# Performance work log

Hardware: AMD Instinct MI355X
Metric: run time of the kernel (lower is better)

The kernel has to match this reference:

```python
import jax, jax.numpy as jnp
import numpy as np

V, E, H, Z = 32000, 512, 1024, 256
B, S, T = 64, 256, 64
BOS_ID, EOS_ID = 1, 2


def gru_cell(x_gates, h, W_hh, b_hh):
    # torch GRU gate order: r, z, n. x_gates: (B,3H) precomputed W_ih@x+b_ih.
    hg = h @ W_hh.T + b_hh
    xr, xz, xn = jnp.split(x_gates, 3, axis=-1)
    hr, hz, hn = jnp.split(hg, 3, axis=-1)
    r = jax.nn.sigmoid(xr + hr)
    z = jax.nn.sigmoid(xz + hz)
    n = jnp.tanh(xn + r * hn)
    return (1.0 - z) * n + z * h


def setup_inputs() -> dict:
    key = jax.random.key(0)
    ks = jax.random.split(key, 24)
    u = lambda k, sh: jax.random.uniform(k, sh, jnp.float32, -0.1, 0.1)
    n = lambda k, sh: jax.random.normal(k, sh, jnp.float32) * 0.05
    inp = {
        'input': jax.random.randint(ks[0], (S, B), 0, V),
        'eps': jax.random.normal(ks[1], (B, Z), jnp.float32),
        'emb_enc': u(ks[2], (V, E)).at[0].set(0.0),  # padding_idx=0
        'Wih_e': n(ks[3], (3 * H, E)), 'Whh_e': n(ks[4], (3 * H, H)),
        'bih_e': n(ks[5], (3 * H,)), 'bhh_e': n(ks[6], (3 * H,)),
        'W_enc': n(ks[7], (Z, H)), 'b_enc': n(ks[8], (Z,)),
        'W_loc': n(ks[9], (Z, Z)), 'b_loc': n(ks[10], (Z,)),
        'W_scale': n(ks[11], (Z, Z)), 'b_scale': n(ks[12], (Z,)),
        'emb_dec': u(ks[13], (V, E)).at[0].set(0.0),
        'W_dec': n(ks[14], (H, Z)), 'b_dec': n(ks[15], (H,)),
        'Wih_d': n(ks[16], (3 * H, E)), 'Whh_d': n(ks[17], (3 * H, H)),
        'bih_d': n(ks[18], (3 * H,)), 'bhh_d': n(ks[19], (3 * H,)),
        'W_voc': n(ks[20], (V, H)), 'b_voc': n(ks[21], (V,)),
    }
    return inp


def reference(input, eps, emb_enc, Wih_e, Whh_e, bih_e, bhh_e,
              W_enc, b_enc, W_loc, b_loc, W_scale, b_scale,
              emb_dec, W_dec, b_dec, Wih_d, Whh_d, bih_d, bhh_d,
              W_voc, b_voc):
    # ---- encode ----
    x = emb_enc[input]                                   # (S,B,E)
    gx = jnp.einsum('sbe,ge->sbg', x, Wih_e) + bih_e     # (S,B,3H)
    h0 = jnp.zeros((B, H), x.dtype)
    h_last, _ = jax.lax.scan(lambda h, g: (gru_cell(g, h, Whh_e, bhh_e), None), h0, gx)
    henc = h_last @ W_enc.T + b_enc                      # (B,Z)
    loc = henc @ W_loc.T + b_loc
    scale = jax.nn.softplus(henc @ W_scale.T + b_scale)
    # ---- reparametrize ----
    z = loc + eps * jnp.exp(0.5 * scale)
    # ---- decode (fixed T steps; original loop is data-dependent on EOS) ----
    hidden = z @ W_dec.T + b_dec                         # (B,H)
    xd = jnp.broadcast_to(emb_dec[EOS_ID], (B, E))       # constant EOS input each step
    gxd = xd @ Wih_d.T + bih_d                           # (B,3H), hoisted out of loop

    def step(h, _):
        h2 = gru_cell(gxd, h, Whh_d, bhh_d)
        log_p = jax.nn.log_softmax(h2 @ W_voc.T + b_voc, axis=-1)  # (B,V)
        tok = jnp.argmax(log_p)  # global flat argmax, as torch.argmax(...).item()
        return h2, (log_p, tok)

    _, (log_p, toks) = jax.lax.scan(step, hidden, None, length=T)
    seq = jnp.concatenate([jnp.array([BOS_ID], toks.dtype), toks])
    return log_p, seq, loc, scale
```

## Files before the change

kernel.cpp:

```cpp
#include <hip/hip_runtime.h>
#include <math.h>
#include <stdint.h>
#include <stddef.h>

typedef unsigned short u16;
typedef unsigned int   u32;
typedef __attribute__((ext_vector_type(8))) short short8;
typedef __attribute__((ext_vector_type(4))) float f32x4;

#define DI __device__ __forceinline__

static constexpr int Vv = 32000, Ee = 512, Hh = 1024, Zz = 256;
static constexpr int Bb = 64, Ss = 256, Tt = 64;
static constexpr int G3 = 3 * Hh;

static constexpr size_t OFF_WHHE  = 0;
static constexpr size_t SZ_WHH    = (size_t)G3 * Hh * 2;
static constexpr size_t OFF_WHHD  = OFF_WHHE + SZ_WHH;
static constexpr size_t OFF_WIHE3 = OFF_WHHD + SZ_WHH;
static constexpr size_t SZ_WIHE3  = (size_t)G3 * (3 * Ee) * 2;
static constexpr size_t OFF_WVOC  = OFF_WIHE3 + SZ_WIHE3;
static constexpr size_t SZ_WVOC   = (size_t)Vv * Hh * 2;
static constexpr size_t OFF_XS    = OFF_WVOC + SZ_WVOC;
static constexpr size_t SZ_XS     = (size_t)Ss * Bb * (3 * Ee) * 2;
static constexpr size_t OFF_GX    = OFF_XS + SZ_XS;
static constexpr size_t SZ_GX     = (size_t)Ss * Bb * G3 * 4;
static constexpr size_t OFF_H2B   = OFF_GX;
static constexpr size_t OFF_H2F   = OFF_GX + SZ_GX;
static constexpr size_t SZ_H2F    = (size_t)Tt * Bb * Hh * 4;
static constexpr size_t OFF_H     = OFF_H2F + SZ_H2F;
static constexpr size_t OFF_GXD   = OFF_H + (size_t)Bb * Hh * 4;
static constexpr size_t OFF_HENC  = OFF_GXD + 12288;
static constexpr size_t OFF_ZB    = OFF_HENC + (size_t)Bb * Zz * 4;
static constexpr size_t OFF_RM    = OFF_ZB + (size_t)Bb * Zz * 4;
static constexpr size_t OFF_SE    = OFF_RM + 16384;
static constexpr size_t OFF_LSE   = OFF_SE + 16384;
static constexpr size_t OFF_BV    = OFF_LSE + 16384;
static constexpr size_t OFF_BI    = OFF_BV + 16384;
static constexpr size_t OFF_CC    = OFF_BI + 16384;
static constexpr size_t OFF_CAND  = OFF_CC + 16384;
static constexpr size_t OFF_BAR   = OFF_CAND + (size_t)4096 * 32 * 4;

static constexpr size_t SZ_HAB    = (size_t)Bb * 2 * Hh * 2;

DI u16 f2bf(float f) {
  u32 u = __float_as_uint(f);
  u32 r = (u + 0x7FFFu + ((u >> 16) & 1u)) >> 16;
  return (u16)r;
}
DI float bf2f(u16 h) { return __uint_as_float(((u32)h) << 16); }

DI f32x4 mfma16(short8 a, short8 b, f32x4 c) {
  return __builtin_amdgcn_mfma_f32_16x16x32_bf16(a, b, c, 0, 0, 0);
}
DI void llds16(const u16* g, u16* l) {
  __builtin_amdgcn_global_load_lds(
      (const __attribute__((address_space(1))) u32*)g,
      (__attribute__((address_space(3))) u32*)l, 16, 0, 0);
}

DI void ag_store_u32(u32* p, u32 v) {
  __hip_atomic_store(p, v, __ATOMIC_RELAXED, __HIP_MEMORY_SCOPE_AGENT);
}
DI u32 ag_load_u32(const u32* p) {
  return __hip_atomic_load((u32*)p, __ATOMIC_RELAXED, __HIP_MEMORY_SCOPE_AGENT);
}
DI void ag_store_f32(float* p, float v) {
  __hip_atomic_store(p, v, __ATOMIC_RELAXED, __HIP_MEMORY_SCOPE_AGENT);
}

DI u16* hbuf_dev(char* rA, char* rB, char* rC, int i) {
  if (i < 192) return (u16*)(rA + (size_t)i * SZ_HAB);
  if (i < 228) return (u16*)(rB + (size_t)(i - 192) * SZ_HAB);
  return (u16*)(rC + (size_t)(i - 228) * SZ_HAB);
}

__global__ void k_zero(u32* p, int n) {
  for (int i = blockIdx.x * 256 + threadIdx.x; i < n; i += gridDim.x * 256) p[i] = 0;
}

__global__ void k_tobf(const float* __restrict__ W, u16* __restrict__ Wb, int n) {
  for (int i = blockIdx.x * 256 + threadIdx.x; i < n; i += gridDim.x * 256) Wb[i] = f2bf(W[i]);
}

__global__ void k_xgather(const int* __restrict__ inp, const float* __restrict__ emb,
                          u16* __restrict__ xs) {
  int n = Ss * Bb * Ee;
  for (int i = blockIdx.x * 256 + threadIdx.x; i < n; i += gridDim.x * 256) {
    int m = i >> 9, k = i & (Ee - 1);
    xs[i] = f2bf(emb[(size_t)inp[m] * Ee + k]);
  }
}

__global__ void k_gxd(const float* __restrict__ emb_dec, const float* __restrict__ Wih_d,
                      const float* __restrict__ bih_d, float* __restrict__ gxd) {
  int g = blockIdx.x * 256 + threadIdx.x;
  if (g >= G3) return;
  const float* er = emb_dec + 2 * Ee;
  const float* wr = Wih_d + (size_t)g * Ee;
  float s = 0.f;
  for (int e = 0; e < Ee; e++) s += er[e] * wr[e];
  gxd[g] = s + bih_d[g];
}

__global__ __launch_bounds__(256, 2) void gemm_bt(
    const u16* __restrict__ A, const u16* __restrict__ Bw, const float* __restrict__ bias,
    float* __restrict__ C, int M, int N, int K) {
  __shared__ __align__(16) u16 As[128 * 32];
  __shared__ __align__(16) u16 Bs[128 * 32];
  int tid = threadIdx.x;
  int wave = tid >> 6, lane = tid & 63;
  int wr = wave >> 1, wc = wave & 1;
  int m0 = blockIdx.y * 128, n0 = blockIdx.x * 128;
  f32x4 acc[4][4];
#pragma unroll
  for (int i = 0; i < 4; i++)
#pragma unroll
    for (int j = 0; j < 4; j++) acc[i][j] = (f32x4){0.f, 0.f, 0.f, 0.f};

  int lrow = lane >> 2, lcol = (lane & 3) * 8;
  int r15 = lane & 15, kk = (lane >> 4) * 8;

  for (int k0 = 0; k0 < K; k0 += 32) {
    __syncthreads();
#pragma unroll
    for (int rch = 0; rch < 2; rch++) {
      int c = rch * 4 + wave;
      int row = c * 16 + lrow;
      llds16(A  + (size_t)(m0 + row) * K + k0 + lcol, &As[c * 512]);
      llds16(Bw + (size_t)(n0 + row) * K + k0 + lcol, &Bs[c * 512]);
    }
    __syncthreads();
    short8 af[4], bfv[4];
#pragma unroll
    for (int mi = 0; mi < 4; mi++)
      af[mi] = *(const short8*)&As[(wr * 64 + mi * 16 + r15) * 32 + kk];
#pragma unroll
    for (int ni = 0; ni < 4; ni++)
      bfv[ni] = *(const short8*)&Bs[(wc * 64 + ni * 16 + r15) * 32 + kk];
#pragma unroll
    for (int mi = 0; mi < 4; mi++)
#pragma unroll
      for (int ni = 0; ni < 4; ni++) acc[mi][ni] = mfma16(af[mi], bfv[ni], acc[mi][ni]);
  }
#pragma unroll
  for (int mi = 0; mi < 4; mi++)
#pragma unroll
    for (int ni = 0; ni < 4; ni++) {
      int col = n0 + wc * 64 + ni * 16 + r15;
      float bs = bias[col];
#pragma unroll
      for (int i = 0; i < 4; i++) {
        int row = m0 + wr * 64 + mi * 16 + (lane >> 4) * 4 + i;
        C[(size_t)row * N + col] = acc[mi][ni][i] + bs;
      }
    }
}

template <int DEC>
__global__ __launch_bounds__(512, 1) void k_pers(
    const u16* __restrict__ W, const float* __restrict__ bhh, const float* __restrict__ gx0,
    char* rA, char* rB, char* rC, float* Hst, float* h2f0, u16* h2b0, u32* bar) {
  int tid = threadIdx.x, wave = tid >> 6, lane = tid & 63;
  int r15 = lane & 15, kk = (lane >> 4) * 8;
  int bq = blockIdx.x & 3, jt = blockIdx.x >> 2;
  int b0 = bq * 16, j0 = jt * 16;
  int kbase = wave * 128;
  const int NSTEP = DEC ? Tt : Ss;

  __shared__ float sC[8][64][13];
  __shared__ float hT[256];
  __shared__ __align__(8) u16 stg[2][16][16];

  int bl = tid >> 4, jc = tid & 15;
  float br = 0.f, bz = 0.f, bn = 0.f;
  float xr = 0.f, xz = 0.f, xn = 0.f;
  if (tid < 256) {
    hT[tid] = DEC ? Hst[(size_t)(b0 + bl) * Hh + j0 + jc] : 0.f;
    int j = j0 + jc;
    br = bhh[j]; bz = bhh[Hh + j]; bn = bhh[2 * Hh + j];
    if (DEC) { xr = gx0[j]; xz = gx0[Hh + j]; xn = gx0[2 * Hh + j]; }
    else {
      const float* gr = gx0 + (size_t)(b0 + bl) * G3;
      xr = gr[j]; xz = gr[Hh + j]; xn = gr[2 * Hh + j];
    }
  }
  __syncthreads();

  const u16* Wrow = W + (size_t)(j0 + r15) * Hh + kbase + kk;
  int lsrc = (bl >> 2) * 16 + jc;
  int isrc = bl & 3;
  int flgidx = (lane * 4 + bq) * 16;

  for (int st = 0; st < NSTEP; st++) {
    const u16* hin = hbuf_dev(rA, rB, rC, st);

    f32x4 acc[3];
#pragma unroll
    for (int g = 0; g < 3; g++) acc[g] = (f32x4){0.f, 0.f, 0.f, 0.f};
    const u16* Ab = hin + (size_t)(b0 + r15) * 2048 + kbase + kk;
#pragma unroll
    for (int ks = 0; ks < 4; ks++) {
      int ko = ks * 32;
      short8 ah = *(const short8*)(Ab + ko);
      short8 al = *(const short8*)(Ab + 1024 + ko);
      short8 w0 = *(const short8*)(Wrow + ko);
      short8 w1 = *(const short8*)(Wrow + (size_t)Hh * Hh + ko);
      short8 w2 = *(const short8*)(Wrow + (size_t)2 * Hh * Hh + ko);
      acc[0] = mfma16(ah, w0, acc[0]);
      acc[1] = mfma16(ah, w1, acc[1]);
      acc[2] = mfma16(ah, w2, acc[2]);
      acc[0] = mfma16(al, w0, acc[0]);
      acc[1] = mfma16(al, w1, acc[1]);
      acc[2] = mfma16(al, w2, acc[2]);
    }
#pragma unroll
    for (int g = 0; g < 3; g++)
#pragma unroll
      for (int i = 0; i < 4; i++) sC[wave][lane][g * 4 + i] = acc[g][i];
    __syncthreads();

    if (tid < 256) {
      float hgr = br, hgz = bz, hgn = bn;
#pragma unroll
      for (int w = 0; w < 8; w++) {
        hgr += sC[w][lsrc][isrc];
        hgz += sC[w][lsrc][4 + isrc];
        hgn += sC[w][lsrc][8 + isrc];
      }
      float rg = 1.0f / (1.0f + expf(-(xr + hgr)));
      float zg = 1.0f / (1.0f + expf(-(xz + hgz)));
      float ng = tanhf(xn + rg * hgn);
      float hn = (1.0f - zg) * ng + zg * hT[tid];
      hT[tid] = hn;
      u16 hi = f2bf(hn), lo = f2bf(hn - bf2f(hi));
      stg[0][bl][jc] = hi;
      stg[1][bl][jc] = lo;
      if (DEC) ag_store_f32(&h2f0[((size_t)st * Bb + b0 + bl) * Hh + j0 + jc], hn);
    }
    __syncthreads();

    if (tid < 256) {
      int part = tid >> 7, idx = tid & 127, row = idx >> 3, dw = idx & 7;
      if (st + 1 < NSTEP) {
        u16* hout = hbuf_dev(rA, rB, rC, st + 1);
        u32 val = ((const u32*)&stg[part][row][0])[dw];
        ag_store_u32((u32*)(hout + (size_t)(b0 + row) * 2048 + part * 1024 + j0) + dw, val);
      }
      if (DEC && tid < 128) {
        u16* h2b = h2b0 + (size_t)st * Bb * Hh;
        ag_store_u32((u32*)(h2b + (size_t)(b0 + row) * Hh + j0) + dw,
                     ((const u32*)&stg[0][row][0])[dw]);
      }
    }

    if (st + 1 < NSTEP) {
      asm volatile("s_waitcnt vmcnt(0)" ::: "memory");
      __syncthreads();
      if (tid == 0)
        ag_store_u32(&bar[blockIdx.x * 16], (u32)(st + 1));
      if (!DEC && tid < 256) {
        const float* gr = gx0 + ((size_t)(st + 1) * Bb + b0 + bl) * G3;
        int j = j0 + jc;
        xr = gr[j]; xz = gr[Hh + j]; xn = gr[2 * Hh + j];
      }
      for (;;) {
        int v = (int)ag_load_u32(&bar[flgidx]);
        if (__all(v >= st + 1)) break;
        __builtin_amdgcn_s_sleep(1);
      }
    }
  }

  if (!DEC && tid < 256)
    Hst[(size_t)(b0 + bl) * Hh + j0 + jc] = hT[tid];
}

template <int DEC>
__global__ __launch_bounds__(512, 1) void k_step3(
    const u16* __restrict__ W, const float* __restrict__ bhh, const float* __restrict__ gxp,
    const u16* __restrict__ hAin, u16* __restrict__ hAout, float* __restrict__ h,
    float* __restrict__ h2f, u16* __restrict__ h2b) {
  __shared__ float sC[4][64][13];
  int tid = threadIdx.x, wave = tid >> 6, lane = tid & 63;
  int mw = wave & 3, khalf = wave >> 2;
  int m0 = mw * 16;
  int r15 = lane & 15, kk = (lane >> 4) * 8;
  int j0 = blockIdx.x * 16;
  int kbase = khalf * 512;

  f32x4 acc[3];
#pragma unroll
  for (int g = 0; g < 3; g++) acc[g] = (f32x4){0.f, 0.f, 0.f, 0.f};

  const u16* Ah = hAin + (size_t)(m0 + r15) * 2048 + kbase + kk;
  const u16* Wr = W + (size_t)(j0 + r15) * Hh + kbase + kk;
#pragma unroll 4
  for (int ks = 0; ks < 16; ks++) {
    int ko = ks * 32;
    short8 ah = *(const short8*)(Ah + ko);
    short8 al = *(const short8*)(Ah + 1024 + ko);
    short8 b0 = *(const short8*)(Wr + ko);
    short8 b1 = *(const short8*)(Wr + (size_t)Hh * Hh + ko);
    short8 b2 = *(const short8*)(Wr + (size_t)2 * Hh * Hh + ko);
    acc[0] = mfma16(ah, b0, acc[0]);
    acc[1] = mfma16(ah, b1, acc[1]);
    acc[2] = mfma16(ah, b2, acc[2]);
    acc[0] = mfma16(al, b0, acc[0]);
    acc[1] = mfma16(al, b1, acc[1]);
    acc[2] = mfma16(al, b2, acc[2]);
  }

  if (khalf == 1) {
#pragma unroll
    for (int g = 0; g < 3; g++)
#pragma unroll
      for (int i = 0; i < 4; i++) sC[mw][lane][g * 4 + i] = acc[g][i];
  }
  __syncthreads();
  if (khalf == 1) return;

  int j = j0 + r15;
  float br = bhh[j], bz = bhh[Hh + j], bn = bhh[2 * Hh + j];
  float xrD = 0.f, xzD = 0.f, xnD = 0.f;
  if (DEC) { xrD = gxp[j]; xzD = gxp[Hh + j]; xnD = gxp[2 * Hh + j]; }
#pragma unroll
  for (int i = 0; i < 4; i++) {
    int b = m0 + (lane >> 4) * 4 + i;
    float hgr = acc[0][i] + sC[mw][lane][i]     + br;
    float hgz = acc[1][i] + sC[mw][lane][4 + i] + bz;
    float hgn = acc[2][i] + sC[mw][lane][8 + i] + bn;
    float xr, xz, xn;
    if (DEC) { xr = xrD; xz = xzD; xn = xnD; }
    else {
      const float* gr = gxp + (size_t)b * G3;
      xr = gr[j]; xz = gr[Hh + j]; xn = gr[2 * Hh + j];
    }
    float rg = 1.0f / (1.0f + expf(-(xr + hgr)));
    float zg = 1.0f / (1.0f + expf(-(xz + hgz)));
    float ng = tanhf(xn + rg * hgn);
    float hold = h[(size_t)b * Hh + j];
    float hn = (1.0f - zg) * ng + zg * hold;
    h[(size_t)b * Hh + j] = hn;
    u16 hi = f2bf(hn);
    u16 lo = f2bf(hn - bf2f(hi));
    hAout[(size_t)b * 2048 + j] = hi;
    hAout[(size_t)b * 2048 + 1024 + j] = lo;
    if (DEC) {
      h2f[(size_t)b * Hh + j] = hn;
      h2b[(size_t)b * Hh + j] = hi;
    }
  }
}

__global__ __launch_bounds__(256, 2) void k_head1(const float* __restrict__ h,
    const float* __restrict__ Wenc, const float* __restrict__ benc, float* __restrict__ henc) {
  int b = blockIdx.x;
  __shared__ float hs[Hh];
  for (int k = threadIdx.x; k < Hh; k += 256) hs[k] = h[(size_t)b * Hh + k];
  __syncthreads();
  int q = threadIdx.x;
  const float* wrw = Wenc + (size_t)q * Hh;
  float s = 0.f;
  for (int k = 0; k < Hh; k++) s += hs[k] * wrw[k];
  henc[b * Zz + q] = s + benc[q];
}

__global__ __launch_bounds__(256, 2) void k_head2(const float* __restrict__ henc,
    const float* __restrict__ Wloc, const float* __restrict__ bloc,
    const float* __restrict__ Wsc, const float* __restrict__ bsc,
    const float* __restrict__ eps, float* __restrict__ outLoc, float* __restrict__ outSc,
    float* __restrict__ zb) {
  int b = blockIdx.x;
  __shared__ float hs[Zz];
  if (threadIdx.x < Zz) hs[threadIdx.x] = henc[b * Zz + threadIdx.x];
  __syncthreads();
  int q = threadIdx.x;
  const float* wl = Wloc + (size_t)q * Zz;
  const float* wsp = Wsc + (size_t)q * Zz;
  float sl = 0.f, ssum = 0.f;
  for (int k = 0; k < Zz; k++) { sl += hs[k] * wl[k]; ssum += hs[k] * wsp[k]; }
  sl += bloc[q]; ssum += bsc[q];
  float sp = fmaxf(ssum, 0.f) + log1pf(expf(-fabsf(ssum)));
  float zv = sl + eps[b * Zz + q] * expf(0.5f * sp);
  outLoc[b * Zz + q] = sl;
  outSc[b * Zz + q] = sp;
  zb[b * Zz + q] = zv;
}

__global__ __launch_bounds__(256, 2) void k_head3(const float* __restrict__ zb,
    const float* __restrict__ Wdec, const float* __restrict__ bdec,
    float* __restrict__ h, u16* __restrict__ hA0) {
  int b = blockIdx.x;
  __shared__ float zs[Zz];
  if (threadIdx.x < Zz) zs[threadIdx.x] = zb[b * Zz + threadIdx.x];
  __syncthreads();
  for (int j = threadIdx.x; j < Hh; j += 256) {
    const float* wrw = Wdec + (size_t)j * Zz;
    float s = 0.f;
    for (int k = 0; k < Zz; k++) s += zs[k] * wrw[k];
    s += bdec[j];
    h[(size_t)b * Hh + j] = s;
    u16 hi = f2bf(s);
    u16 lo = f2bf(s - bf2f(hi));
    hA0[(size_t)b * 2048 + j] = hi;
    hA0[(size_t)b * 2048 + 1024 + j] = lo;
  }
}

__global__ __launch_bounds__(1024, 1) void k_soft(
    float* __restrict__ logits, const float* __restrict__ h2f,
    const float* __restrict__ Wvoc, const float* __restrict__ bvoc,
    float* __restrict__ bestv, int* __restrict__ besti) {
  __shared__ float row[Vv];
  __shared__ float hrow[Hh];
  __shared__ float red[16];
  __shared__ float srm, ssum, slse;
  __shared__ int lcnt, scc;
  __shared__ int lcand[32];
  __shared__ float lex[32], del[32];
  int r = blockIdx.x;
  int tid = threadIdx.x, wave = tid >> 6, lane = tid & 63;
  float* grow = logits + (size_t)r * Vv;
  if (tid == 0) lcnt = 0;
  hrow[tid] = h2f[(size_t)r * Hh + tid];
  float m = -3.0e38f;
  for (int c = tid * 4; c < Vv; c += 4096) {
    f32x4 v = *(const f32x4*)(grow + c);
    *(f32x4*)(row + c) = v;
    m = fmaxf(fmaxf(m, v.x), fmaxf(v.y, fmaxf(v.z, v.w)));
  }
  for (int o = 32; o; o >>= 1) m = fmaxf(m, __shfl_xor(m, o));
  if (lane == 0) red[wave] = m;
  __syncthreads();
  if (tid == 0) {
    float t = red[0];
    for (int i = 1; i < 16; i++) t = fmaxf(t, red[i]);
    srm = t;
  }
  __syncthreads();
  float rm = srm;
  float s = 0.f;
  for (int c = tid * 4; c < Vv; c += 4096) {
    f32x4 v = *(const f32x4*)(row + c);
    s += expf(v.x - rm) + expf(v.y - rm) + expf(v.z - rm) + expf(v.w - rm);
    if (v.x >= rm - 0.0625f) { int sl = atomicAdd(&lcnt, 1); if (sl < 32) lcand[sl] = c; }
    if (v.y >= rm - 0.0625f) { int sl = atomicAdd(&lcnt, 1); if (sl < 32) lcand[sl] = c + 1; }
    if (v.z >= rm - 0.0625f) { int sl = atomicAdd(&lcnt, 1); if (sl < 32) lcand[sl] = c + 2; }
    if (v.w >= rm - 0.0625f) { int sl = atomicAdd(&lcnt, 1); if (sl < 32) lcand[sl] = c + 3; }
  }
  for (int o = 32; o; o >>= 1) s += __shfl_xor(s, o);
  if (lane == 0) red[wave] = s;
  __syncthreads();
  if (tid == 0) {
    float t = 0.f;
    for (int i = 0; i < 16; i++) t += red[i];
    ssum = t;
    int cc = lcnt < 32 ? lcnt : 32;
    for (int i = 0; i < cc; i++)
      for (int k2 = i + 1; k2 < cc; k2++)
        if (lcand[k2] < lcand[i]) { int q = lcand[i]; lcand[i] = lcand[k2]; lcand[k2] = q; }
    scc = cc;
  }
  __syncthreads();
  int cnt = scc;
  for (int ci = wave; ci < cnt; ci += 16) {
    int v = lcand[ci];
    const float* wrw = Wvoc + (size_t)v * Hh;
    float sd = 0.f;
    for (int k = lane; k < Hh; k += 64) sd += hrow[k] * wrw[k];
    for (int o = 32; o; o >>= 1) sd += __shfl_xor(sd, o);
    if (lane == 0) {
      float le = sd + bvoc[v];
      lex[ci] = le;
      del[ci] = expf(le - rm) - expf(row[v] - rm);
    }
  }
  __syncthreads();
  if (tid == 0) {
    float se = ssum;
    for (int i = 0; i < cnt; i++) se += del[i];
    float lse = rm + logf(se);
    slse = lse;
    float bv = -3.0e38f; int bvi = 0;
    for (int i = 0; i < cnt; i++)
      if (lex[i] > bv) { bv = lex[i]; bvi = lcand[i]; }
    bestv[r] = bv - lse;
    besti[r] = (r & 63) * Vv + bvi;
  }
  __syncthreads();
  float l = slse;
  for (int c = tid * 4; c < Vv; c += 4096) {
    f32x4 v = *(const f32x4*)(row + c);
    v.x -= l; v.y -= l; v.z -= l; v.w -= l;
    *(f32x4*)(grow + c) = v;
  }
}

__global__ void k_argmax(const float* __restrict__ bestv, const int* __restrict__ besti,
                         float* __restrict__ outseq) {
  int tid = threadIdx.x;
  if (tid == 0) outseq[0] = 1.0f;
  for (int t = 0; t < Tt; t++) {
    float v = bestv[t * 64 + tid];
    int ii = besti[t * 64 + tid];
    for (int o = 1; o < 64; o <<= 1) {
      float ov = __shfl_xor(v, o);
      int oi = __shfl_xor(ii, o);
      if (ov > v || (ov == v && oi < ii)) { v = ov; ii = oi; }
    }
    if (tid == 0) outseq[1 + t] = (float)ii;
  }
}

extern "C" void kernel_launch(void* const* d_in, const int* in_sizes, int n_in,
                              void* d_out, int out_size, void* d_ws, size_t ws_size,
                              hipStream_t stream) {
  (void)in_sizes; (void)n_in; (void)out_size; (void)ws_size;
  const int*   inp     = (const int*)d_in[0];
  const float* eps     = (const float*)d_in[1];
  const float* emb_enc = (const float*)d_in[2];
  const float* Wih_e   = (const float*)d_in[3];
  const float* Whh_e   = (const float*)d_in[4];
  const float* bih_e   = (const float*)d_in[5];
  const float* bhh_e   = (const float*)d_in[6];
  const float* W_enc   = (const float*)d_in[7];
  const float* b_enc   = (const float*)d_in[8];
  const float* W_loc   = (const float*)d_in[9];
  const float* b_loc   = (const float*)d_in[10];
  const float* W_sc    = (const float*)d_in[11];
  const float* b_sc    = (const float*)d_in[12];
  const float* emb_dec = (const float*)d_in[13];
  const float* W_dec   = (const float*)d_in[14];
  const float* b_dec   = (const float*)d_in[15];
  const float* Wih_d   = (const float*)d_in[16];
  const float* Whh_d   = (const float*)d_in[17];
  const float* bih_d   = (const float*)d_in[18];
  const float* bhh_d   = (const float*)d_in[19];
  const float* W_voc   = (const float*)d_in[20];
  const float* b_voc   = (const float*)d_in[21];

  char* ws = (char*)d_ws;
  u16*   WHHE  = (u16*)(ws + OFF_WHHE);
  u16*   WHHD  = (u16*)(ws + OFF_WHHD);
  u16*   WIHB  = (u16*)(ws + OFF_WIHE3);
  u16*   WVOC  = (u16*)(ws + OFF_WVOC);
  u16*   XS    = (u16*)(ws + OFF_XS);
  float* GX    = (float*)(ws + OFF_GX);
  float* Hst   = (float*)(ws + OFF_H);
  float* H2F   = (float*)(ws + OFF_H2F);
  u16*   H2B   = (u16*)(ws + OFF_H2B);
  float* GXD   = (float*)(ws + OFF_GXD);
  float* HENC  = (float*)(ws + OFF_HENC);
  float* ZB    = (float*)(ws + OFF_ZB);
  float* BV    = (float*)(ws + OFF_BV);
  int*   BI    = (int*)(ws + OFF_BI);
  u32*   BAR   = (u32*)(ws + OFF_BAR);

  char* rA = ws + OFF_XS;
  char* rB = ws + OFF_WIHE3;
  char* rC = ws + OFF_H2F;
  auto hbuf = [&](int i) -> u16* {
    if (i < 192) return (u16*)(rA + (size_t)i * SZ_HAB);
    if (i < 228) return (u16*)(rB + (size_t)(i - 192) * SZ_HAB);
    return (u16*)(rC + (size_t)(i - 228) * SZ_HAB);
  };

  float* out     = (float*)d_out;
  float* logits  = out;
  float* outseq  = out + (size_t)Tt * Bb * Vv;
  float* outloc  = outseq + (Tt + 1);
  float* outsc   = outloc + Bb * Zz;

  k_tobf<<<1024, 256, 0, stream>>>(Whh_e, WHHE, G3 * Hh);
  k_tobf<<<1024, 256, 0, stream>>>(Whh_d, WHHD, G3 * Hh);
  k_tobf<<<512, 256, 0, stream>>>(Wih_e, WIHB, G3 * Ee);
  k_tobf<<<2048, 256, 0, stream>>>(W_voc, WVOC, Vv * Hh);
  k_xgather<<<2048, 256, 0, stream>>>(inp, emb_enc, XS);

  {
    dim3 g(G3 / 128, (Ss * Bb) / 128);
    gemm_bt<<<g, 256, 0, stream>>>(XS, WIHB, bih_e, GX, Ss * Bb, G3, Ee);
  }
  k_gxd<<<12, 256, 0, stream>>>(emb_dec, Wih_d, bih_d, GXD);
  k_zero<<<64, 256, 0, stream>>>((u32*)hbuf(0), (int)(SZ_HAB / 4));
  k_zero<<<1, 256, 0, stream>>>(BAR, 4096);

  hipError_t ce;
  {
    const u16* a0 = WHHE; const float* a1 = bhh_e; const float* a2 = GX;
    char* a3 = rA; char* a4 = rB; char* a5 = rC; float* a6 = Hst;
    float* a7 = nullptr; u16* a8 = nullptr; u32* a9 = BAR;
    void* args[] = {&a0,&a1,&a2,&a3,&a4,&a5,&a6,&a7,&a8,&a9};
    ce = hipLaunchCooperativeKernel(reinterpret_cast<void*>(&k_pers<0>),
                                    dim3(256), dim3(512), args, 0, stream);
  }
  if (ce != hipSuccess) {
    for (int s = 0; s < Ss; s++)
      k_step3<0><<<64, 512, 0, stream>>>(WHHE, bhh_e, GX + (size_t)s * Bb * G3,
                                         hbuf(s), hbuf(s + 1), Hst, nullptr, nullptr);
  }

  k_head1<<<64, 256, 0, stream>>>(Hst, W_enc, b_enc, HENC);
  k_head2<<<64, 256, 0, stream>>>(HENC, W_loc, b_loc, W_sc, b_sc, eps, outloc, outsc, ZB);
  k_head3<<<64, 256, 0, stream>>>(ZB, W_dec, b_dec, Hst, hbuf(0));
  k_zero<<<1, 256, 0, stream>>>(BAR, 4096);

  {
    const u16* a0 = WHHD; const float* a1 = bhh_d; const float* a2 = GXD;
    char* a3 = rA; char* a4 = rB; char* a5 = rC; float* a6 = Hst;
    float* a7 = H2F; u16* a8 = H2B; u32* a9 = BAR;
    void* args[] = {&a0,&a1,&a2,&a3,&a4,&a5,&a6,&a7,&a8,&a9};
    hipError_t cd = hipLaunchCooperativeKernel(reinterpret_cast<void*>(&k_pers<1>),
                                               dim3(256), dim3(512), args, 0, stream);
    if (cd != hipSuccess) {
      for (int t = 0; t < Tt; t++)
        k_step3<1><<<64, 512, 0, stream>>>(WHHD, bhh_d, GXD, hbuf(t), hbuf(t + 1), Hst,
                                           H2F + (size_t)t * Bb * Hh,
                                           H2B + (size_t)t * Bb * Hh);
    }
  }

  {
    dim3 g(Vv / 128, (Tt * Bb) / 128);
    gemm_bt<<<g, 256, 0, stream>>>(H2B, WVOC, b_voc, logits, Tt * Bb, Vv, Hh);
  }

  k_soft<<<Tt * Bb, 1024, 0, stream>>>(logits, H2F, W_voc, b_voc, BV, BI);
  k_argmax<<<1, 64, 0, stream>>>(BV, BI, outseq);
}
```

Before: 2.637 ms.

## Group vocab GEMM tiles for L2 reuse, drop LDS row cache in softmax, single-wave barrier poll

The vocab projection now runs as a new grouped-tile GEMM. Each run of consecutive blocks covers all M tiles for a group of 5 N tiles, so W_voc tiles are reused from L2 across the 32 row tiles. The softmax kernel no longer stages the 32000-float logits row in shared memory and instead re-reads it from global memory, which cuts LDS use so more blocks can be resident per CU. In the persistent GRU kernel, only wave 0 now spins on the grid barrier flag and the other waves wait at a block-level sync, which reduces polling traffic.

Result: faster. 2.576 ms (-2.3%).

```diff
diff --git a/kernel.cpp b/kernel.cpp
--- a/kernel.cpp
+++ b/kernel.cpp
@@ -32,14 +32,9 @@
 static constexpr size_t OFF_GXD   = OFF_H + (size_t)Bb * Hh * 4;
 static constexpr size_t OFF_HENC  = OFF_GXD + 12288;
 static constexpr size_t OFF_ZB    = OFF_HENC + (size_t)Bb * Zz * 4;
-static constexpr size_t OFF_RM    = OFF_ZB + (size_t)Bb * Zz * 4;
-static constexpr size_t OFF_SE    = OFF_RM + 16384;
-static constexpr size_t OFF_LSE   = OFF_SE + 16384;
-static constexpr size_t OFF_BV    = OFF_LSE + 16384;
+static constexpr size_t OFF_BV    = OFF_ZB + (size_t)Bb * Zz * 4;
 static constexpr size_t OFF_BI    = OFF_BV + 16384;
-static constexpr size_t OFF_CC    = OFF_BI + 16384;
-static constexpr size_t OFF_CAND  = OFF_CC + 16384;
-static constexpr size_t OFF_BAR   = OFF_CAND + (size_t)4096 * 32 * 4;
+static constexpr size_t OFF_BAR   = OFF_BI + 16384;
 
 static constexpr size_t SZ_HAB    = (size_t)Bb * 2 * Hh * 2;
 
@@ -112,6 +107,65 @@
   int wave = tid >> 6, lane = tid & 63;
   int wr = wave >> 1, wc = wave & 1;
   int m0 = blockIdx.y * 128, n0 = blockIdx.x * 128;
+  f32x4 acc[4][4];
+#pragma unroll
+  for (int i = 0; i < 4; i++)
+#pragma unroll
+    for (int j = 0; j < 4; j++) acc[i][j] = (f32x4){0.f, 0.f, 0.f, 0.f};
+
+  int lrow = lane >> 2, lcol = (lane & 3) * 8;
+  int r15 = lane & 15, kk = (lane >> 4) * 8;
+
+  for (int k0 = 0; k0 < K; k0 += 32) {
+    __syncthreads();
+#pragma unroll
+    for (int rch = 0; rch < 2; rch++) {
+      int c = rch * 4 + wave;
+      int row = c * 16 + lrow;
+      llds16(A  + (size_t)(m0 + row) * K + k0 + lcol, &As[c * 512]);
+      llds16(Bw + (size_t)(n0 + row) * K + k0 + lcol, &Bs[c * 512]);
+    }
+    __syncthreads();
+    short8 af[4], bfv[4];
+#pragma unroll
+    for (int mi = 0; mi < 4; mi++)
+      af[mi] = *(const short8*)&As[(wr * 64 + mi * 16 + r15) * 32 + kk];
+#pragma unroll
+    for (int ni = 0; ni < 4; ni++)
+      bfv[ni] = *(const short8*)&Bs[(wc * 64 + ni * 16 + r15) * 32 + kk];
+#pragma unroll
+    for (int mi = 0; mi < 4; mi++)
+#pragma unroll
+      for (int ni = 0; ni < 4; ni++) acc[mi][ni] = mfma16(af[mi], bfv[ni], acc[mi][ni]);
+  }
+#pragma unroll
+  for (int mi = 0; mi < 4; mi++)
+#pragma unroll
+    for (int ni = 0; ni < 4; ni++) {
+      int col = n0 + wc * 64 + ni * 16 + r15;
+      float bs = bias[col];
+#pragma unroll
+      for (int i = 0; i < 4; i++) {
+        int row = m0 + wr * 64 + mi * 16 + (lane >> 4) * 4 + i;
+        C[(size_t)row * N + col] = acc[mi][ni][i] + bs;
+      }
+    }
+}
+
+__global__ __launch_bounds__(256, 2) void gemm_grp(
+    const u16* __restrict__ A, const u16* __restrict__ Bw, const float* __restrict__ bias,
+    float* __restrict__ C, int M, int N, int K, int GN) {
+  __shared__ __align__(16) u16 As[128 * 32];
+  __shared__ __align__(16) u16 Bs[128 * 32];
+  int tid = threadIdx.x;
+  int wave = tid >> 6, lane = tid & 63;
+  int wr = wave >> 1, wc = wave & 1;
+  int mp = M >> 7;
+  int perg = mp * GN;
+  int grp = blockIdx.x / perg;
+  int rem = blockIdx.x - grp * perg;
+  int m0 = (rem / GN) * 128;
+  int n0 = (grp * GN + rem % GN) * 128;
   f32x4 acc[4][4];
 #pragma unroll
   for (int i = 0; i < 4; i++)
@@ -264,11 +318,14 @@
         int j = j0 + jc;
         xr = gr[j]; xz = gr[Hh + j]; xn = gr[2 * Hh + j];
       }
-      for (;;) {
-        int v = (int)ag_load_u32(&bar[flgidx]);
-        if (__all(v >= st + 1)) break;
-        __builtin_amdgcn_s_sleep(1);
+      if (wave == 0) {
+        for (;;) {
+          int v = (int)ag_load_u32(&bar[flgidx]);
+          if (__all(v >= st + 1)) break;
+          __builtin_amdgcn_s_sleep(1);
+        }
       }
+      __syncthreads();
     }
   }
 
@@ -408,11 +465,10 @@
   }
 }
 
-__global__ __launch_bounds__(1024, 1) void k_soft(
+__global__ __launch_bounds__(1024, 8) void k_soft(
     float* __restrict__ logits, const float* __restrict__ h2f,
     const float* __restrict__ Wvoc, const float* __restrict__ bvoc,
     float* __restrict__ bestv, int* __restrict__ besti) {
-  __shared__ float row[Vv];
   __shared__ float hrow[Hh];
   __shared__ float red[16];
   __shared__ float srm, ssum, slse;
@@ -427,7 +483,6 @@
   float m = -3.0e38f;
   for (int c = tid * 4; c < Vv; c += 4096) {
     f32x4 v = *(const f32x4*)(grow + c);
-    *(f32x4*)(row + c) = v;
     m = fmaxf(fmaxf(m, v.x), fmaxf(v.y, fmaxf(v.z, v.w)));
   }
   for (int o = 32; o; o >>= 1) m = fmaxf(m, __shfl_xor(m, o));
@@ -442,7 +497,7 @@
   float rm = srm;
   float s = 0.f;
   for (int c = tid * 4; c < Vv; c += 4096) {
-    f32x4 v = *(const f32x4*)(row + c);
+    f32x4 v = *(const f32x4*)(grow + c);
     s += expf(v.x - rm) + expf(v.y - rm) + expf(v.z - rm) + expf(v.w - rm);
     if (v.x >= rm - 0.0625f) { int sl = atomicAdd(&lcnt, 1); if (sl < 32) lcand[sl] = c; }
     if (v.y >= rm - 0.0625f) { int sl = atomicAdd(&lcnt, 1); if (sl < 32) lcand[sl] = c + 1; }
@@ -473,7 +528,7 @@
     if (lane == 0) {
       float le = sd + bvoc[v];
       lex[ci] = le;
-      del[ci] = expf(le - rm) - expf(row[v] - rm);
+      del[ci] = expf(le - rm) - expf(grow[v] - rm);
     }
   }
   __syncthreads();
@@ -491,7 +546,7 @@
   __syncthreads();
   float l = slse;
   for (int c = tid * 4; c < Vv; c += 4096) {
-    f32x4 v = *(const f32x4*)(row + c);
+    f32x4 v = *(const f32x4*)(grow + c);
     v.x -= l; v.y -= l; v.z -= l; v.w -= l;
     *(f32x4*)(grow + c) = v;
   }
@@ -621,10 +676,7 @@
     }
   }
 
-  {
-    dim3 g(Vv / 128, (Tt * Bb) / 128);
-    gemm_bt<<<g, 256, 0, stream>>>(H2B, WVOC, b_voc, logits, Tt * Bb, Vv, Hh);
-  }
+  gemm_grp<<<8000, 256, 0, stream>>>(H2B, WVOC, b_voc, logits, Tt * Bb, Vv, Hh, 5);
 
   k_soft<<<Tt * Bb, 1024, 0, stream>>>(logits, H2F, W_voc, b_voc, BV, BI);
   k_argmax<<<1, 64, 0, stream>>>(BV, BI, outseq);
```
